# Performance work log

Measured on AMD Instinct MI355X. Metric: run time of the kernel, lower is better.

## Reference

```python
import jax, jax.numpy as jnp
import numpy as np
import math

N, E = 50000, 800000
NFEAT, HID, NCLASS = 512, 96, 64
NUM_LAYERS = 8
ALPHA, THETA = 0.1, 0.5


def setup_inputs() -> dict:
    key = jax.random.key(0)
    ks = jax.random.split(key, 8)
    x = jax.random.normal(ks[0], (N, NFEAT), dtype=jnp.float32)
    # dense_to_sparse(adj_t) -> edge_index; weights are discarded by the module,
    # so propagation uses unit edge weights. We generate the edge list directly.
    edge_index = jax.random.randint(ks[1], (2, E), 0, N, dtype=jnp.int32)
    s_in = 1.0 / math.sqrt(NFEAT)
    s_hid = 1.0 / math.sqrt(HID)
    W_in = jax.random.uniform(ks[2], (NFEAT, HID), jnp.float32, -s_in, s_in)
    b_in = jax.random.uniform(ks[3], (HID,), jnp.float32, -s_in, s_in)
    conv_W = jax.random.uniform(ks[4], (NUM_LAYERS, HID, HID), jnp.float32, -s_hid, s_hid)
    W_out = jax.random.uniform(ks[5], (HID, NCLASS), jnp.float32, -s_hid, s_hid)
    b_out = jax.random.uniform(ks[6], (NCLASS,), jnp.float32, -s_hid, s_hid)
    return {"x": x, "edge_index": edge_index, "W_in": W_in, "b_in": b_in,
            "conv_W": conv_W, "W_out": W_out, "b_out": b_out}


def reference(x, edge_index, W_in, b_in, conv_W, W_out, b_out):
    # Eval mode: dropout is identity.
    src, dst = edge_index[0], edge_index[1]
    h = jax.nn.relu(x @ W_in + b_in)          # [N, HID]
    x0 = h
    for layer in range(NUM_LAYERS):
        beta = math.log(THETA / (layer + 1) + 1.0)
        # sparse propagation: out[i] = sum over edges (j -> i) of h[j]
        agg = jax.ops.segment_sum(h[src], dst, num_segments=N)   # [N, HID]
        hc = (1.0 - ALPHA) * agg + ALPHA * x0                    # initial residual
        h = jax.nn.relu((1.0 - beta) * hc + beta * (hc @ conv_W[layer]))
    out = h @ W_out + b_out                   # [N, NCLASS]
    return jax.nn.log_softmax(out, axis=-1)
```

## Files before the change

### kernel.cpp

```cpp
#include <hip/hip_runtime.h>
#include <hip/hip_bf16.h>
#include <math.h>

#define N_NODES 50000
#define N_EDGES 800000
#define NFEAT   512
#define HID     96
#define NCLASS  64
#define NUM_LAYERS 8
#define ALPHA   0.1f
#define NSB     49
#define NBB     196
#define R1      16667
#define R2      33334

typedef __attribute__((ext_vector_type(8))) short short8;
typedef __attribute__((ext_vector_type(4))) float f32x4;

__device__ __forceinline__ unsigned short f2bf(float f) {
    unsigned int u = __float_as_uint(f);
    unsigned int r = u + 0x7FFF + ((u >> 16) & 1);
    return (unsigned short)(r >> 16);
}
__device__ __forceinline__ unsigned cvtpk(float a, float b) {
    __hip_bfloat162 h = __float22bfloat162_rn(float2{a, b});
    return *reinterpret_cast<unsigned*>(&h);
}
__device__ __forceinline__ float bflo(unsigned int u) { return __uint_as_float(u << 16); }
__device__ __forceinline__ float bfhi(unsigned int u) { return __uint_as_float(u & 0xFFFF0000u); }
__device__ __forceinline__ float bf2f(short s) {
    return __uint_as_float(((unsigned int)(unsigned short)s) << 16);
}

__device__ __forceinline__ void gload16(const float* g, float* l) {
    __builtin_amdgcn_global_load_lds(
        (const __attribute__((address_space(1))) void*)g,
        (__attribute__((address_space(3))) void*)l, 16, 0, 0);
}

__device__ __forceinline__ int src_range(int s) {
    return (s >= R2) ? 2 : (s >= R1 ? 1 : 0);
}

__global__ void hist_kernel(const int* __restrict__ src, const int* __restrict__ dst,
                            unsigned* __restrict__ degpack) {
    int e = blockIdx.x * blockDim.x + threadIdx.x;
    if (e < N_EDGES) {
        int r = src_range(src[e]);
        atomicAdd(&degpack[dst[e]], 1u << (10 * r));
    }
}

__global__ void scan1_kernel(const unsigned* __restrict__ degpack,
                             int* __restrict__ deg, int* __restrict__ row_start,
                             int* __restrict__ blk_sum) {
    __shared__ int sd[1024];
    int t = threadIdx.x;
    int i = blockIdx.x * 1024 + t;
    unsigned p = (i < N_NODES) ? degpack[i] : 0u;
    int dt = (int)((p & 1023u) + ((p >> 10) & 1023u) + ((p >> 20) & 1023u));
    int v = (i < N_NODES) ? ((dt + 3) & ~3) : 0;
    sd[t] = v;
    __syncthreads();
    for (int off = 1; off < 1024; off <<= 1) {
        int tv = (t >= off) ? sd[t - off] : 0;
        __syncthreads();
        sd[t] += tv;
        __syncthreads();
    }
    if (i < N_NODES) {
        row_start[i] = sd[t] - v;
        deg[i] = dt;
    }
    if (t == 1023) blk_sum[blockIdx.x] = sd[1023];
}

__global__ void scan3_kernel(int* __restrict__ row_start, const int* __restrict__ blk_sum,
                             const int* __restrict__ deg, const unsigned* __restrict__ degpack,
                             int* __restrict__ rsub, int* __restrict__ csr_src) {
    __shared__ int soff;
    int t = threadIdx.x;
    if (t < 64) {
        int v = (t < blockIdx.x) ? blk_sum[t] : 0;
#pragma unroll
        for (int off = 1; off < 64; off <<= 1) v += __shfl_xor(v, off);
        if (t == 0) soff = v;
    }
    __syncthreads();
    int i = blockIdx.x * 1024 + t;
    if (i < N_NODES) {
        int rs = row_start[i] + soff;
        row_start[i] = rs;
        int d = deg[i], pd = (d + 3) & ~3;
        for (int p = d; p < pd; p++) csr_src[rs + p] = N_NODES;
        unsigned pk = degpack[i];
        int dr0 = (int)(pk & 1023u), dr1 = (int)((pk >> 10) & 1023u);
        rsub[i]               = rs;
        rsub[N_NODES + i]     = rs + dr0;
        rsub[2 * N_NODES + i] = rs + dr0 + dr1;
    }
}

__global__ void fill_kernel(const int* __restrict__ src, const int* __restrict__ dst,
                            const int* __restrict__ rsub, unsigned* __restrict__ cursorpack,
                            int* __restrict__ csr_src) {
    int e = blockIdx.x * blockDim.x + threadIdx.x;
    if (e < N_EDGES) {
        int s = src[e], d = dst[e];
        int r = src_range(s);
        unsigned old = atomicAdd(&cursorpack[d], 1u << (10 * r));
        int cnt = (int)((old >> (10 * r)) & 1023u);
        csr_src[rsub[r * N_NODES + d] + cnt] = s;
    }
}

__global__ __launch_bounds__(256) void bin_hist2_kernel(
        const int* __restrict__ deg, int* __restrict__ node_rank,
        int* __restrict__ blk_bin_cnt) {
    __shared__ int lh[64];
    int t = threadIdx.x;
    if (t < 64) lh[t] = 0;
    __syncthreads();
    int n = blockIdx.x * 256 + t;
    if (n < N_NODES) {
        int nq = (deg[n] + 3) >> 2; if (nq > 63) nq = 63;
        node_rank[n] = atomicAdd(&lh[nq], 1);
    }
    __syncthreads();
    if (t < 64) blk_bin_cnt[blockIdx.x * 64 + t] = lh[t];
}

__global__ void bin_offsets_kernel(const int* __restrict__ blk_bin_cnt,
                                   int* __restrict__ blk_bin_off,
                                   int* __restrict__ bin_base) {
    __shared__ int tot[64];
    int b = threadIdx.x;
    int acc = 0;
    for (int blk = 0; blk < NBB; blk++) {
        blk_bin_off[blk * 64 + b] = acc;
        acc += blk_bin_cnt[blk * 64 + b];
    }
    tot[b] = acc;
    __syncthreads();
    if (b == 0) {
        int a = 0;
        for (int i = 63; i >= 0; i--) { bin_base[i] = a; a += tot[i]; }
    }
}

__global__ __launch_bounds__(256) void bin_place_kernel(
        const int* __restrict__ deg, const int* __restrict__ node_rank,
        const int* __restrict__ blk_bin_off, const int* __restrict__ bin_base,
        int* __restrict__ perm) {
    int n = blockIdx.x * 256 + threadIdx.x;
    if (n < N_NODES) {
        int nq = (deg[n] + 3) >> 2; if (nq > 63) nq = 63;
        perm[bin_base[nq] + blk_bin_off[blockIdx.x * 64 + nq] + node_rank[n]] = n;
    }
}

__global__ void convert_win_kernel(const float* __restrict__ W, short* __restrict__ Wt) {
    int t = blockIdx.x * 256 + threadIdx.x;
    int lane = t & 63;
    int n    = (t >> 6) % 6;
    int ks   = t / 384;
    int quad = lane >> 4, l16 = lane & 15;
    short8 v;
#pragma unroll
    for (int j = 0; j < 8; j++)
        v[j] = (short)f2bf(W[(size_t)(ks * 32 + quad * 8 + j) * HID + n * 16 + l16]);
    *(short8*)&Wt[(size_t)t * 8] = v;
}

__global__ void convert_wout_kernel(const float* __restrict__ W, short* __restrict__ Wt,
                                    short* __restrict__ h0, short* __restrict__ hb,
                                    short* __restrict__ hc) {
    int n = blockIdx.x;
    int k = threadIdx.x;
    Wt[(size_t)n * HID + k] = (short)f2bf(W[(size_t)k * NCLASS + n]);
    if (n == 0) {
        h0[(size_t)N_NODES * HID + k] = 0;
        hb[(size_t)N_NODES * HID + k] = 0;
        hc[(size_t)N_NODES * HID + k] = 0;
    }
}

__global__ void convert_wconv_kernel(const float* __restrict__ W, short* __restrict__ Wc) {
    int n = blockIdx.x;
    int l = blockIdx.y;
    int k = threadIdx.x;
    Wc[(size_t)l * HID * HID + (size_t)n * HID + k] =
        (short)f2bf(W[(size_t)l * HID * HID + (size_t)k * HID + n]);
}

__global__ __launch_bounds__(256) void gemm_in_kernel(
        const float* __restrict__ x, const short* __restrict__ WtT,
        const float* __restrict__ b, short* __restrict__ h0) {
    __shared__ __align__(16) float As[2][4096];
    int tid  = threadIdx.x;
    int wave = tid >> 6, lane = tid & 63;
    int quad = lane >> 4, l16 = lane & 15;
    int row0 = blockIdx.x * 64;

    const float* gsrc[4];
#pragma unroll
    for (int r = 0; r < 4; r++) {
        int rl  = r * 4 + (lane >> 4);
        int row = row0 + wave * 16 + rl;
        if (row >= N_NODES) row = N_NODES - 1;
        int c2s = (lane & 15) ^ rl;
        gsrc[r] = &x[(size_t)row * NFEAT + c2s * 4];
    }

    f32x4 acc[6];
#pragma unroll
    for (int n = 0; n < 6; n++) acc[n] = (f32x4){0.f, 0.f, 0.f, 0.f};

    float* lb0 = &As[0][wave * 1024];
    float* lb1 = &As[1][wave * 1024];
#pragma unroll
    for (int r = 0; r < 4; r++) gload16(gsrc[r], lb0 + r * 256);

#pragma unroll
    for (int c = 0; c < 8; c++) {
        if (c < 7) {
            float* nb = ((c + 1) & 1) ? lb1 : lb0;
#pragma unroll
            for (int r = 0; r < 4; r++) gload16(gsrc[r] + (c + 1) * 64, nb + r * 256);
            asm volatile("s_waitcnt vmcnt(4)" ::: "memory");
        } else {
            asm volatile("s_waitcnt vmcnt(0)" ::: "memory");
        }
        __builtin_amdgcn_sched_barrier(0);
        const float* cb = ((c & 1) ? lb1 : lb0) + l16 * 64;
#pragma unroll
        for (int s = 0; s < 2; s++) {
            int c2a = s * 8 + quad * 2;
            f32x4 fa = *(const f32x4*)&cb[((c2a    ) ^ l16) * 4];
            f32x4 fb = *(const f32x4*)&cb[((c2a + 1) ^ l16) * 4];
            union { short8 sv; uint4 u; } af;
            af.u.x = cvtpk(fa[0], fa[1]);
            af.u.y = cvtpk(fa[2], fa[3]);
            af.u.z = cvtpk(fb[0], fb[1]);
            af.u.w = cvtpk(fb[2], fb[3]);
            int ks = c * 2 + s;
            const short* bbase = &WtT[(size_t)(ks * 6) * 512 + lane * 8];
#pragma unroll
            for (int n = 0; n < 6; n++) {
                short8 bfrag = *(const short8*)&bbase[n * 512];
                acc[n] = __builtin_amdgcn_mfma_f32_16x16x32_bf16(af.sv, bfrag, acc[n], 0, 0, 0);
            }
        }
    }

    int row0w = row0 + wave * 16;
#pragma unroll
    for (int n = 0; n < 6; n++) {
        int col = n * 16 + l16;
        float bias = b[col];
#pragma unroll
        for (int r = 0; r < 4; r++) {
            int grow = row0w + quad * 4 + r;
            if (grow < N_NODES) {
                float v = acc[n][r] + bias;
                v = v > 0.f ? v : 0.f;
                h0[(size_t)grow * HID + col] = (short)f2bf(v);
            }
        }
    }
}

__global__ __launch_bounds__(384) void layer_kernel(
        const short* __restrict__ h_in, const short* __restrict__ x0bf,
        const int* __restrict__ row_start, const int* __restrict__ deg,
        const int* __restrict__ csr_src, const int* __restrict__ perm,
        const short* __restrict__ Wc, float beta, short* __restrict__ h_out) {
    __shared__ short As[32][104];
    __shared__ int   snode[32];
    int tid = threadIdx.x;
    int tx = tid % 12;
    int ty = tid / 12;
    int idx = blockIdx.x * 32 + ty;
    bool valid = idx < N_NODES;
    int node = valid ? perm[idx] : (N_NODES - 1);
    if (tx == 0) snode[ty] = valid ? node : -1;

    int s = row_start[node];
    int d = deg[node];
    int nq = (d + 3) >> 2;
    const int4* c4 = (const int4*)(csr_src + s);
    uint4 xq = *(const uint4*)&x0bf[(size_t)node * HID + tx * 8];

    float acc[8];
#pragma unroll
    for (int j = 0; j < 8; j++) acc[j] = 0.f;
    int4 nv = {N_NODES, N_NODES, N_NODES, N_NODES};
    if (nq > 0) nv = c4[0];
    for (int i = 0; i < nq; i++) {
        int4 iv = nv;
        if (i + 1 < nq) nv = c4[i + 1];
        uint4 a0 = *(const uint4*)&h_in[(size_t)iv.x * HID + tx * 8];
        uint4 a1 = *(const uint4*)&h_in[(size_t)iv.y * HID + tx * 8];
        uint4 a2 = *(const uint4*)&h_in[(size_t)iv.z * HID + tx * 8];
        uint4 a3 = *(const uint4*)&h_in[(size_t)iv.w * HID + tx * 8];
        acc[0] += bflo(a0.x) + bflo(a1.x) + bflo(a2.x) + bflo(a3.x);
        acc[1] += bfhi(a0.x) + bfhi(a1.x) + bfhi(a2.x) + bfhi(a3.x);
        acc[2] += bflo(a0.y) + bflo(a1.y) + bflo(a2.y) + bflo(a3.y);
        acc[3] += bfhi(a0.y) + bfhi(a1.y) + bfhi(a2.y) + bfhi(a3.y);
        acc[4] += bflo(a0.z) + bflo(a1.z) + bflo(a2.z) + bflo(a3.z);
        acc[5] += bfhi(a0.z) + bfhi(a1.z) + bfhi(a2.z) + bfhi(a3.z);
        acc[6] += bflo(a0.w) + bflo(a1.w) + bflo(a2.w) + bflo(a3.w);
        acc[7] += bfhi(a0.w) + bfhi(a1.w) + bfhi(a2.w) + bfhi(a3.w);
    }
    float hc[8];
    hc[0] = (1.f - ALPHA) * acc[0] + ALPHA * bflo(xq.x);
    hc[1] = (1.f - ALPHA) * acc[1] + ALPHA * bfhi(xq.x);
    hc[2] = (1.f - ALPHA) * acc[2] + ALPHA * bflo(xq.y);
    hc[3] = (1.f - ALPHA) * acc[3] + ALPHA * bfhi(xq.y);
    hc[4] = (1.f - ALPHA) * acc[4] + ALPHA * bflo(xq.z);
    hc[5] = (1.f - ALPHA) * acc[5] + ALPHA * bfhi(xq.z);
    hc[6] = (1.f - ALPHA) * acc[6] + ALPHA * bflo(xq.w);
    hc[7] = (1.f - ALPHA) * acc[7] + ALPHA * bfhi(xq.w);
    {
        uint4 pk;
        pk.x = cvtpk(hc[0], hc[1]);
        pk.y = cvtpk(hc[2], hc[3]);
        pk.z = cvtpk(hc[4], hc[5]);
        pk.w = cvtpk(hc[6], hc[7]);
        *(uint4*)&As[ty][tx * 8] = pk;
    }
    __syncthreads();

    int wave = tid >> 6, lane = tid & 63;
    int quad = lane >> 4, l16 = lane & 15;
    int rt = wave & 1;
    int ct0 = (wave >> 1) * 2, ct1 = ct0 + 1;

    f32x4 g0 = (f32x4){0.f,0.f,0.f,0.f}, g1 = (f32x4){0.f,0.f,0.f,0.f};
#pragma unroll
    for (int ks = 0; ks < 3; ks++) {
        short8 afrag = *(const short8*)&As[rt * 16 + l16][ks * 32 + quad * 8];
        short8 b0 = *(const short8*)&Wc[(size_t)(ct0 * 16 + l16) * HID + ks * 32 + quad * 8];
        short8 b1 = *(const short8*)&Wc[(size_t)(ct1 * 16 + l16) * HID + ks * 32 + quad * 8];
        g0 = __builtin_amdgcn_mfma_f32_16x16x32_bf16(afrag, b0, g0, 0, 0, 0);
        g1 = __builtin_amdgcn_mfma_f32_16x16x32_bf16(afrag, b1, g1, 0, 0, 0);
    }
    float ob = 1.0f - beta;
#pragma unroll
    for (int r = 0; r < 4; r++) {
        int lrow = rt * 16 + quad * 4 + r;
        int nd = snode[lrow];
        if (nd >= 0) {
            int c0 = ct0 * 16 + l16;
            int c1 = ct1 * 16 + l16;
            float v0 = ob * bf2f(As[lrow][c0]) + beta * g0[r];
            float v1 = ob * bf2f(As[lrow][c1]) + beta * g1[r];
            v0 = v0 > 0.f ? v0 : 0.f;
            v1 = v1 > 0.f ? v1 : 0.f;
            h_out[(size_t)nd * HID + c0] = (short)f2bf(v0);
            h_out[(size_t)nd * HID + c1] = (short)f2bf(v1);
        }
    }
}

__global__ __launch_bounds__(256) void out_kernel(
        const short* __restrict__ h_bf, const short* __restrict__ Wt,
        const float* __restrict__ b, float* __restrict__ out) {
    int tid = threadIdx.x;
    int wave = tid >> 6, lane = tid & 63;
    int quad = lane >> 4, l16 = lane & 15;
    int row0 = blockIdx.x * 64 + wave * 16;

    f32x4 acc[4];
#pragma unroll
    for (int n = 0; n < 4; n++) acc[n] = (f32x4){0.f, 0.f, 0.f, 0.f};

    int arow = row0 + l16; if (arow > N_NODES) arow = N_NODES;
#pragma unroll
    for (int ks = 0; ks < 3; ks++) {
        short8 afrag = *(const short8*)&h_bf[(size_t)arow * HID + ks * 32 + quad * 8];
#pragma unroll
        for (int n = 0; n < 4; n++) {
            short8 bfrag = *(const short8*)&Wt[(size_t)(n * 16 + l16) * HID + ks * 32 + quad * 8];
            acc[n] = __builtin_amdgcn_mfma_f32_16x16x32_bf16(afrag, bfrag, acc[n], 0, 0, 0);
        }
    }
#pragma unroll
    for (int n = 0; n < 4; n++) {
        float bias = b[n * 16 + l16];
#pragma unroll
        for (int r = 0; r < 4; r++) acc[n][r] += bias;
    }
#pragma unroll
    for (int r = 0; r < 4; r++) {
        float m = acc[0][r];
        m = fmaxf(m, acc[1][r]); m = fmaxf(m, acc[2][r]); m = fmaxf(m, acc[3][r]);
#pragma unroll
        for (int off = 1; off < 16; off <<= 1) m = fmaxf(m, __shfl_xor(m, off));
        float s = __expf(acc[0][r] - m) + __expf(acc[1][r] - m)
                + __expf(acc[2][r] - m) + __expf(acc[3][r] - m);
#pragma unroll
        for (int off = 1; off < 16; off <<= 1) s += __shfl_xor(s, off);
        float lse = m + __logf(s);
        int grow = row0 + quad * 4 + r;
        if (grow < N_NODES) {
#pragma unroll
            for (int n = 0; n < 4; n++)
                out[(size_t)grow * NCLASS + n * 16 + l16] = acc[n][r] - lse;
        }
    }
}

extern "C" void kernel_launch(void* const* d_in, const int* in_sizes, int n_in,
                              void* d_out, int out_size, void* d_ws, size_t ws_size,
                              hipStream_t stream) {
    const float* x      = (const float*)d_in[0];
    const int*   ei     = (const int*)d_in[1];
    const int*   srcp   = ei;
    const int*   dstp   = ei + N_EDGES;
    const float* W_in   = (const float*)d_in[2];
    const float* b_in   = (const float*)d_in[3];
    const float* conv_W = (const float*)d_in[4];
    const float* W_out  = (const float*)d_in[5];
    const float* b_out  = (const float*)d_in[6];
    float* out = (float*)d_out;

    short* h0  = (short*)d_ws;
    short* h_b = h0  + (size_t)(N_NODES + 1) * HID;
    short* h_c = h_b + (size_t)(N_NODES + 1) * HID;
    short* Wt_in  = h_c + (size_t)(N_NODES + 1) * HID;
    short* Wt_out = Wt_in + (size_t)HID * NFEAT;
    short* Wc     = Wt_out + (size_t)NCLASS * HID;
    unsigned* degpack    = (unsigned*)(Wc + (size_t)NUM_LAYERS * HID * HID);
    unsigned* cursorpack = degpack + N_NODES;
    int* deg        = (int*)(cursorpack + N_NODES);
    int* row_start  = deg + N_NODES;
    int* rsub       = row_start + N_NODES;
    int* blk_sum    = rsub + 3 * N_NODES;
    int* bin_base   = blk_sum + 64;
    int* node_rank  = bin_base + 64;
    int* perm       = node_rank + N_NODES;
    int* blk_bin_cnt= perm + N_NODES;
    int* blk_bin_off= blk_bin_cnt + NBB * 64;
    int* csr_src    = blk_bin_off + NBB * 64;

    hipMemsetAsync(degpack, 0, 2 * N_NODES * sizeof(unsigned), stream);
    hist_kernel<<<(N_EDGES + 255) / 256, 256, 0, stream>>>(srcp, dstp, degpack);
    scan1_kernel<<<NSB, 1024, 0, stream>>>(degpack, deg, row_start, blk_sum);
    scan3_kernel<<<NSB, 1024, 0, stream>>>(row_start, blk_sum, deg, degpack, rsub, csr_src);
    fill_kernel<<<(N_EDGES + 255) / 256, 256, 0, stream>>>(srcp, dstp, rsub, cursorpack, csr_src);
    bin_hist2_kernel<<<NBB, 256, 0, stream>>>(deg, node_rank, blk_bin_cnt);
    bin_offsets_kernel<<<1, 64, 0, stream>>>(blk_bin_cnt, blk_bin_off, bin_base);
    bin_place_kernel<<<NBB, 256, 0, stream>>>(deg, node_rank, blk_bin_off, bin_base, perm);

    convert_win_kernel<<<24, 256, 0, stream>>>(W_in, Wt_in);
    convert_wout_kernel<<<NCLASS, HID, 0, stream>>>(W_out, Wt_out, h0, h_b, h_c);
    convert_wconv_kernel<<<dim3(HID, NUM_LAYERS), HID, 0, stream>>>(conv_W, Wc);
    gemm_in_kernel<<<(N_NODES + 63) / 64, 256, 0, stream>>>(x, Wt_in, b_in, h0);

    short* cur = h0;
    short* nxt = h_b;
    for (int l = 0; l < NUM_LAYERS; l++) {
        float beta = logf(0.5f / (float)(l + 1) + 1.0f);
        layer_kernel<<<(N_NODES + 31) / 32, 384, 0, stream>>>(
            cur, h0, row_start, deg, csr_src, perm, Wc + (size_t)l * HID * HID, beta, nxt);
        cur = nxt;
        nxt = (cur == h_b) ? h_c : h_b;
    }

    out_kernel<<<(N_NODES + 63) / 64, 256, 0, stream>>>(cur, Wt_out, b_out, out);
}
```

Before: 508.6 us.

## Replace atomic CSR fill with two-pass bucket partition and LDS-atomic placement

```diff
diff --git a/kernel.cpp b/kernel.cpp
--- a/kernel.cpp
+++ b/kernel.cpp
@@ -13,6 +13,8 @@
 #define NBB     196
 #define R1      16667
 #define R2      33334
+#define NBKT    49
+#define BCAP    20480
 
 typedef __attribute__((ext_vector_type(8))) short short8;
 typedef __attribute__((ext_vector_type(4))) float f32x4;
@@ -101,16 +103,66 @@
     }
 }
 
-__global__ void fill_kernel(const int* __restrict__ src, const int* __restrict__ dst,
-                            const int* __restrict__ rsub, unsigned* __restrict__ cursorpack,
-                            int* __restrict__ csr_src) {
-    int e = blockIdx.x * blockDim.x + threadIdx.x;
-    if (e < N_EDGES) {
-        int s = src[e], d = dst[e];
+__global__ __launch_bounds__(256) void partition_kernel(
+        const int* __restrict__ src, const int* __restrict__ dst,
+        int* __restrict__ bkt_cnt, unsigned* __restrict__ bkt) {
+    __shared__ int lh[NBKT], gb[NBKT];
+    int t = threadIdx.x;
+    if (t < NBKT) lh[t] = 0;
+    __syncthreads();
+    int e0 = blockIdx.x * 2048;
+    int pv[8], bv[8];
+#pragma unroll
+    for (int k = 0; k < 8; k++) {
+        int e = e0 + k * 256 + t;
+        bool ok = e < N_EDGES;
+        int s = ok ? src[e] : 0;
+        int d = ok ? dst[e] : 0;
+        bv[k] = ok ? (d >> 10) : -1;
+        pv[k] = (s << 10) | (d & 1023);
+        if (ok) atomicAdd(&lh[d >> 10], 1);
+    }
+    __syncthreads();
+    if (t < NBKT) {
+        int c = lh[t];
+        gb[t] = c ? atomicAdd(&bkt_cnt[t], c) : 0;
+        lh[t] = 0;
+    }
+    __syncthreads();
+#pragma unroll
+    for (int k = 0; k < 8; k++) {
+        int b = bv[k];
+        if (b >= 0) {
+            int rank = atomicAdd(&lh[b], 1);
+            bkt[(size_t)b * BCAP + gb[b] + rank] = (unsigned)pv[k];
+        }
+    }
+}
+
+__global__ __launch_bounds__(256) void place_kernel(
+        const unsigned* __restrict__ bkt, const int* __restrict__ bkt_cnt,
+        const int* __restrict__ rsub, int* __restrict__ csr_src) {
+    __shared__ int cur[1024 * 3];
+    int b = blockIdx.x, t = threadIdx.x;
+    int n0 = b << 10;
+    for (int ln = t; ln < 1024; ln += 256) {
+        int node = n0 + ln;
+        if (node < N_NODES) {
+#pragma unroll
+            for (int r = 0; r < 3; r++)
+                cur[ln * 3 + r] = rsub[r * N_NODES + node];
+        }
+    }
+    __syncthreads();
+    int cnt = bkt_cnt[b];
+    const unsigned* bp = &bkt[(size_t)b * BCAP];
+    for (int i = t; i < cnt; i += 256) {
+        unsigned p = bp[i];
+        int s  = (int)(p >> 10);
+        int ln = (int)(p & 1023u);
         int r = src_range(s);
-        unsigned old = atomicAdd(&cursorpack[d], 1u << (10 * r));
-        int cnt = (int)((old >> (10 * r)) & 1023u);
-        csr_src[rsub[r * N_NODES + d] + cnt] = s;
+        int pos = atomicAdd(&cur[ln * 3 + r], 1);
+        csr_src[pos] = s;
     }
 }
 
@@ -431,9 +483,9 @@
     short* Wt_in  = h_c + (size_t)(N_NODES + 1) * HID;
     short* Wt_out = Wt_in + (size_t)HID * NFEAT;
     short* Wc     = Wt_out + (size_t)NCLASS * HID;
-    unsigned* degpack    = (unsigned*)(Wc + (size_t)NUM_LAYERS * HID * HID);
-    unsigned* cursorpack = degpack + N_NODES;
-    int* deg        = (int*)(cursorpack + N_NODES);
+    unsigned* degpack = (unsigned*)(Wc + (size_t)NUM_LAYERS * HID * HID);
+    int* bkt_cnt    = (int*)(degpack + N_NODES);
+    int* deg        = bkt_cnt + 64;
     int* row_start  = deg + N_NODES;
     int* rsub       = row_start + N_NODES;
     int* blk_sum    = rsub + 3 * N_NODES;
@@ -442,13 +494,15 @@
     int* perm       = node_rank + N_NODES;
     int* blk_bin_cnt= perm + N_NODES;
     int* blk_bin_off= blk_bin_cnt + NBB * 64;
-    int* csr_src    = blk_bin_off + NBB * 64;
-
-    hipMemsetAsync(degpack, 0, 2 * N_NODES * sizeof(unsigned), stream);
+    unsigned* bkt   = (unsigned*)(blk_bin_off + NBB * 64);
+    int* csr_src    = (int*)(bkt + (size_t)NBKT * BCAP);
+
+    hipMemsetAsync(degpack, 0, (N_NODES + 64) * sizeof(unsigned), stream);
     hist_kernel<<<(N_EDGES + 255) / 256, 256, 0, stream>>>(srcp, dstp, degpack);
     scan1_kernel<<<NSB, 1024, 0, stream>>>(degpack, deg, row_start, blk_sum);
     scan3_kernel<<<NSB, 1024, 0, stream>>>(row_start, blk_sum, deg, degpack, rsub, csr_src);
-    fill_kernel<<<(N_EDGES + 255) / 256, 256, 0, stream>>>(srcp, dstp, rsub, cursorpack, csr_src);
+    partition_kernel<<<(N_EDGES + 2047) / 2048, 256, 0, stream>>>(srcp, dstp, bkt_cnt, bkt);
+    place_kernel<<<NBKT, 256, 0, stream>>>(bkt, bkt_cnt, rsub, csr_src);
     bin_hist2_kernel<<<NBB, 256, 0, stream>>>(deg, node_rank, blk_bin_cnt);
     bin_offsets_kernel<<<1, 64, 0, stream>>>(blk_bin_cnt, blk_bin_off, bin_base);
     bin_place_kernel<<<NBB, 256, 0, stream>>>(deg, node_rank, blk_bin_off, bin_base, perm);
```

New measurement: 496.9 us. 1.02x faster.
